# Kernel optimization log

Measured on AMD Instinct MI355X. Metric: run time of the kernel, lower is better.

Reference implementation:

```python
import jax, jax.numpy as jnp
import numpy as np

B, DIN, DOUT = 4096, 4096, 4096

def setup_inputs() -> dict:
    key = jax.random.key(0)
    k1, k2, k3 = jax.random.split(key, 3)
    x = jax.random.normal(k1, (B, DIN), dtype=jnp.float32)
    W = jax.random.normal(k2, (DOUT, DIN), dtype=jnp.float32) * 0.01
    alpha = jnp.ones((DOUT, DIN), dtype=jnp.float32) * 0.01
    eta = jnp.asarray(0.1, dtype=jnp.float32)
    bias = jnp.zeros((DOUT,), dtype=jnp.float32)
    return {"x": x, "W": W, "alpha": alpha, "eta": eta, "bias": bias}

def reference(x, W, alpha, eta, bias):
    # y_slow = x @ W.T + b                          (B, DOUT)
    y_slow = jnp.einsum('bi,oi->bo', x, W) + bias
    # x_norm = x / (||x|| + 1e-8)
    x_norm = x / (jnp.linalg.norm(x, axis=-1, keepdims=True) + 1e-8)
    y_pre = jnp.tanh(y_slow)
    # plastic_i = eta * y_pre_i * sum_j sigmoid(alpha)_ij * x_norm_j * x_j
    # (algebraic rewrite of bmm over per-sample outer-product trace; same math)
    s = jnp.einsum('bi,oi->bo', x_norm * x, jax.nn.sigmoid(alpha))  # (B, DOUT)
    plastic = eta * y_pre * s
    return y_slow + plastic
```

## Files before the change

### kernel.cpp

```cpp
#include <hip/hip_runtime.h>
#include <hip/hip_bf16.h>
#include <math.h>


typedef __attribute__((ext_vector_type(4))) float floatx4;
typedef __attribute__((ext_vector_type(8))) short shortx8;

#define MAT_N 4096
#define MAT_ELEMS ((size_t)MAT_N * MAT_N)

__device__ __forceinline__ unsigned short f2bf(float f) {
    unsigned int u = __float_as_uint(f);
    unsigned int r = (u + 0x7fffu + ((u >> 16) & 1u)) >> 16;
    return (unsigned short)r;
}

__device__ __forceinline__ void gload_lds16(const void* gptr, void* lptr) {
    __builtin_amdgcn_global_load_lds(
        (const __attribute__((address_space(1))) unsigned int*)gptr,
        (__attribute__((address_space(3))) unsigned int*)lptr,
        16, 0, 0);
}

__global__ __launch_bounds__(512) void convx_kernel(const float* __restrict__ x,
                                                    unsigned short* __restrict__ xb,
                                                    unsigned char* __restrict__ p8,
                                                    float* __restrict__ sumsq) {
    size_t base = ((size_t)blockIdx.x * 512 + threadIdx.x) * 8;
    const float4* xp = (const float4*)(x + base);
    float4 a = xp[0], b = xp[1];
    float v[8] = {a.x, a.y, a.z, a.w, b.x, b.y, b.z, b.w};
    shortx8 xo;
    float sq[8];
    float s = 0.f;
#pragma unroll
    for (int j = 0; j < 8; j++) {
        xo[j] = (short)f2bf(v[j]);
        sq[j] = v[j] * v[j];
        s += sq[j];
    }
    *(shortx8*)(xb + base) = xo;
    int p0 = __builtin_amdgcn_cvt_pk_fp8_f32(sq[0], sq[1], 0, false);
    p0 = __builtin_amdgcn_cvt_pk_fp8_f32(sq[2], sq[3], p0, true);
    int p1 = __builtin_amdgcn_cvt_pk_fp8_f32(sq[4], sq[5], 0, false);
    p1 = __builtin_amdgcn_cvt_pk_fp8_f32(sq[6], sq[7], p1, true);
    int2 pv = {p0, p1};
    *(int2*)(p8 + base) = pv;
    for (int off = 32; off > 0; off >>= 1) s += __shfl_down(s, off, 64);
    if ((threadIdx.x & 63) == 0) atomicAdd(&sumsq[base >> 12], s);
}

__global__ __launch_bounds__(512) void convwa_kernel(const float* __restrict__ W,
                                                     const float* __restrict__ alpha,
                                                     unsigned short* __restrict__ wb,
                                                     unsigned char* __restrict__ a8) {
    size_t base = ((size_t)blockIdx.x * 512 + threadIdx.x) * 8;
    const float4* wp = (const float4*)(W + base);
    const float4* ap = (const float4*)(alpha + base);
    float4 w0 = wp[0], w1 = wp[1], a0 = ap[0], a1 = ap[1];
    float wv[8] = {w0.x, w0.y, w0.z, w0.w, w1.x, w1.y, w1.z, w1.w};
    float av[8] = {a0.x, a0.y, a0.z, a0.w, a1.x, a1.y, a1.z, a1.w};
    shortx8 wo;
    float sg[8];
#pragma unroll
    for (int j = 0; j < 8; j++) {
        wo[j] = (short)f2bf(wv[j]);
        sg[j] = 1.0f / (1.0f + __expf(-av[j]));
    }
    *(shortx8*)(wb + base) = wo;
    int p0 = __builtin_amdgcn_cvt_pk_fp8_f32(sg[0], sg[1], 0, false);
    p0 = __builtin_amdgcn_cvt_pk_fp8_f32(sg[2], sg[3], p0, true);
    int p1 = __builtin_amdgcn_cvt_pk_fp8_f32(sg[4], sg[5], 0, false);
    p1 = __builtin_amdgcn_cvt_pk_fp8_f32(sg[6], sg[7], p1, true);
    int2 pv = {p0, p1};
    *(int2*)(a8 + base) = pv;
}

__global__ __launch_bounds__(512, 4) void fused_gemm_kernel(
    const unsigned short* __restrict__ X,
    const unsigned short* __restrict__ Wb,
    const unsigned char* __restrict__ P8,
    const unsigned char* __restrict__ A8,
    const float* __restrict__ bias,
    const float* __restrict__ eta_p,
    const float* __restrict__ sumsq,
    float* __restrict__ out) {
    constexpr int K = MAT_N;
    constexpr int N = MAT_N;
    __shared__ __align__(16) unsigned short sX[128 * 64];
    __shared__ __align__(16) unsigned short sW[128 * 64];
    __shared__ __align__(16) unsigned char  sP[128 * 64];
    __shared__ __align__(16) unsigned char  sA[128 * 64];

    const int tid = threadIdx.x;
    const int row0 = blockIdx.y * 128;
    const int col0 = blockIdx.x * 128;
    const int lane = tid & 63;
    const int wave = tid >> 6;
    const int wm = (wave >> 1) * 32;
    const int wn = (wave & 1) * 64;
    const int quad = lane >> 4;
    const int l16 = lane & 15;

    floatx4 accY[2][4], accS[2][4];
#pragma unroll
    for (int i = 0; i < 2; i++)
#pragma unroll
        for (int j = 0; j < 4; j++) {
            accY[i][j] = (floatx4){0.f, 0.f, 0.f, 0.f};
            accS[i][j] = (floatx4){0.f, 0.f, 0.f, 0.f};
        }

    const int row_s = tid >> 3;
    const int kc_g  = (tid & 7) ^ (row_s & 7);
    const size_t arow = (size_t)(row0 + row_s) * K + kc_g * 8;
    const size_t brow = (size_t)(col0 + row_s) * K + kc_g * 8;
    const int r8 = tid >> 2;
    const int slot8 = (2 * (tid & 3)) ^ (r8 & 6);
    const size_t prow = (size_t)(row0 + r8) * K + slot8 * 8;
    const size_t qrow = (size_t)(col0 + r8) * K + slot8 * 8;

    for (int k0 = 0; k0 < K; k0 += 64) {
#pragma unroll
        for (int i = 0; i < 2; i++) {
            const size_t go = (size_t)i * 64 * K + k0;
            const int lo = i * 4096 + tid * 8;
            gload_lds16(X + arow + go, sX + lo);
            gload_lds16(Wb + brow + go, sW + lo);
        }
        gload_lds16(P8 + prow + k0, sP + tid * 16);
        gload_lds16(A8 + qrow + k0, sA + tid * 16);
        __syncthreads();

#pragma unroll
        for (int s = 0; s < 2; s++) {
            const int kcp = ((s * 4 + quad) ^ (l16 & 7)) * 8;
            const int lsp = ((s * 4 + quad) ^ (l16 & 6)) * 8;
            {
                shortx8 af[2], bfr[4];
#pragma unroll
                for (int i = 0; i < 2; i++)
                    af[i] = *(const shortx8*)(sX + (wm + i * 16 + l16) * 64 + kcp);
#pragma unroll
                for (int j = 0; j < 4; j++)
                    bfr[j] = *(const shortx8*)(sW + (wn + j * 16 + l16) * 64 + kcp);
#pragma unroll
                for (int i = 0; i < 2; i++)
#pragma unroll
                    for (int j = 0; j < 4; j++)
                        accY[i][j] = __builtin_amdgcn_mfma_f32_16x16x32_bf16(af[i], bfr[j], accY[i][j], 0, 0, 0);
            }
            {
                long ap[2], bp[4];
#pragma unroll
                for (int i = 0; i < 2; i++)
                    ap[i] = *(const long*)(sP + (wm + i * 16 + l16) * 64 + lsp);
#pragma unroll
                for (int j = 0; j < 4; j++)
                    bp[j] = *(const long*)(sA + (wn + j * 16 + l16) * 64 + lsp);
#pragma unroll
                for (int i = 0; i < 2; i++)
#pragma unroll
                    for (int j = 0; j < 4; j++)
                        accS[i][j] = __builtin_amdgcn_mfma_f32_16x16x32_fp8_fp8(ap[i], bp[j], accS[i][j], 0, 0, 0);
            }
        }
        __syncthreads();
    }

    const float eta = *eta_p;
#pragma unroll
    for (int i = 0; i < 2; i++) {
#pragma unroll
        for (int r = 0; r < 4; r++) {
            const int grow = row0 + wm + i * 16 + quad * 4 + r;
            const float invn = 1.0f / (sqrtf(sumsq[grow]) + 1e-8f);
#pragma unroll
            for (int j = 0; j < 4; j++) {
                const int gcol = col0 + wn + j * 16 + l16;
                float y = accY[i][j][r] + bias[gcol];
                float s = accS[i][j][r] * invn;
                out[(size_t)grow * N + gcol] = y + eta * tanhf(y) * s;
            }
        }
    }
}

extern "C" void kernel_launch(void* const* d_in, const int* in_sizes, int n_in,
                              void* d_out, int out_size, void* d_ws, size_t ws_size,
                              hipStream_t stream) {
    const float* x     = (const float*)d_in[0];
    const float* W     = (const float*)d_in[1];
    const float* alpha = (const float*)d_in[2];
    const float* eta   = (const float*)d_in[3];
    const float* bias  = (const float*)d_in[4];
    float* out = (float*)d_out;

    char* ws = (char*)d_ws;
    float* sumsq = (float*)ws;
    unsigned short* xb = (unsigned short*)(ws + 16384);
    unsigned short* wb = xb + MAT_ELEMS;
    unsigned char*  p8 = (unsigned char*)(wb + MAT_ELEMS);
    unsigned char*  a8 = p8 + MAT_ELEMS;

    hipMemsetAsync(sumsq, 0, MAT_N * sizeof(float), stream);
    convx_kernel<<<MAT_ELEMS / (8 * 512), 512, 0, stream>>>(x, xb, p8, sumsq);
    convwa_kernel<<<MAT_ELEMS / (8 * 512), 512, 0, stream>>>(W, alpha, wb, a8);

    dim3 grid(MAT_N / 128, MAT_N / 128);
    fused_gemm_kernel<<<grid, 512, 0, stream>>>(xb, wb, p8, a8, bias, eta, sumsq, out);
}
```

Before: 466.3 us.

## Fold row norm into fp8 operand and permute fp8 layout for wide LDS reads

The x conversion kernel becomes one block per row. It computes the row norm itself and writes x^2/||x|| into the fp8 buffer, which removes the memset, the atomics and the per-row normalization in the GEMM epilogue. The fp8 operands are stored with a permuted 8-byte chunk order so each lane fetches both k-substeps in one 16-byte LDS read, replacing two 8-byte reads. Pre-scaling by the inverse norm before fp8 quantization changes rounding behaviour. The new packing drops the previous XOR swizzle, which may add LDS bank conflicts.

```diff
diff --git a/kernel.cpp b/kernel.cpp
--- a/kernel.cpp
+++ b/kernel.cpp
@@ -5,6 +5,7 @@
 
 typedef __attribute__((ext_vector_type(4))) float floatx4;
 typedef __attribute__((ext_vector_type(8))) short shortx8;
+typedef __attribute__((ext_vector_type(2))) long longx2;
 
 #define MAT_N 4096
 #define MAT_ELEMS ((size_t)MAT_N * MAT_N)
@@ -13,6 +14,11 @@
     unsigned int u = __float_as_uint(f);
     unsigned int r = (u + 0x7fffu + ((u >> 16) & 1u)) >> 16;
     return (unsigned short)r;
+}
+
+__device__ __forceinline__ int pack_fp8x4(float a, float b, float c, float d) {
+    int p = __builtin_amdgcn_cvt_pk_fp8_f32(a, b, 0, false);
+    return __builtin_amdgcn_cvt_pk_fp8_f32(c, d, p, true);
 }
 
 __device__ __forceinline__ void gload_lds16(const void* gptr, void* lptr) {
@@ -22,39 +28,55 @@
         16, 0, 0);
 }
 
-__global__ __launch_bounds__(512) void convx_kernel(const float* __restrict__ x,
+__device__ __forceinline__ int perm8(int c) { return ((c & 3) << 1) | (c >> 2); }
+
+__global__ __launch_bounds__(256) void convx_kernel(const float* __restrict__ x,
                                                     unsigned short* __restrict__ xb,
-                                                    unsigned char* __restrict__ p8,
-                                                    float* __restrict__ sumsq) {
-    size_t base = ((size_t)blockIdx.x * 512 + threadIdx.x) * 8;
-    const float4* xp = (const float4*)(x + base);
-    float4 a = xp[0], b = xp[1];
-    float v[8] = {a.x, a.y, a.z, a.w, b.x, b.y, b.z, b.w};
-    shortx8 xo;
-    float sq[8];
+                                                    unsigned char* __restrict__ p8) {
+    const int row = blockIdx.x;
+    const int t = threadIdx.x;
+    const float* xr = x + (size_t)row * MAT_N;
+    float v[2][8];
     float s = 0.f;
 #pragma unroll
-    for (int j = 0; j < 8; j++) {
-        xo[j] = (short)f2bf(v[j]);
-        sq[j] = v[j] * v[j];
-        s += sq[j];
-    }
-    *(shortx8*)(xb + base) = xo;
-    int p0 = __builtin_amdgcn_cvt_pk_fp8_f32(sq[0], sq[1], 0, false);
-    p0 = __builtin_amdgcn_cvt_pk_fp8_f32(sq[2], sq[3], p0, true);
-    int p1 = __builtin_amdgcn_cvt_pk_fp8_f32(sq[4], sq[5], 0, false);
-    p1 = __builtin_amdgcn_cvt_pk_fp8_f32(sq[6], sq[7], p1, true);
-    int2 pv = {p0, p1};
-    *(int2*)(p8 + base) = pv;
+    for (int h = 0; h < 2; h++) {
+        const float4* p = (const float4*)(xr + (t + h * 256) * 8);
+        float4 a = p[0], b = p[1];
+        v[h][0] = a.x; v[h][1] = a.y; v[h][2] = a.z; v[h][3] = a.w;
+        v[h][4] = b.x; v[h][5] = b.y; v[h][6] = b.z; v[h][7] = b.w;
+#pragma unroll
+        for (int j = 0; j < 8; j++) s += v[h][j] * v[h][j];
+    }
     for (int off = 32; off > 0; off >>= 1) s += __shfl_down(s, off, 64);
-    if ((threadIdx.x & 63) == 0) atomicAdd(&sumsq[base >> 12], s);
+    __shared__ float red[4];
+    if ((t & 63) == 0) red[t >> 6] = s;
+    __syncthreads();
+    const float inv = 1.0f / (sqrtf(red[0] + red[1] + red[2] + red[3]) + 1e-8f);
+    unsigned short* xrow = xb + (size_t)row * MAT_N;
+    unsigned char* prow = p8 + (size_t)row * MAT_N;
+#pragma unroll
+    for (int h = 0; h < 2; h++) {
+        const int c = t + h * 256;
+        shortx8 xo;
+        float q[8];
+#pragma unroll
+        for (int j = 0; j < 8; j++) {
+            xo[j] = (short)f2bf(v[h][j]);
+            q[j] = v[h][j] * v[h][j] * inv;
+        }
+        *(shortx8*)(xrow + c * 8) = xo;
+        int2 pv = {pack_fp8x4(q[0], q[1], q[2], q[3]),
+                   pack_fp8x4(q[4], q[5], q[6], q[7])};
+        *(int2*)(prow + (c & ~7) * 8 + perm8(c & 7) * 8) = pv;
+    }
 }
 
 __global__ __launch_bounds__(512) void convwa_kernel(const float* __restrict__ W,
                                                      const float* __restrict__ alpha,
                                                      unsigned short* __restrict__ wb,
                                                      unsigned char* __restrict__ a8) {
-    size_t base = ((size_t)blockIdx.x * 512 + threadIdx.x) * 8;
+    const size_t c = (size_t)blockIdx.x * 512 + threadIdx.x;
+    const size_t base = c * 8;
     const float4* wp = (const float4*)(W + base);
     const float4* ap = (const float4*)(alpha + base);
     float4 w0 = wp[0], w1 = wp[1], a0 = ap[0], a1 = ap[1];
@@ -68,12 +90,9 @@
         sg[j] = 1.0f / (1.0f + __expf(-av[j]));
     }
     *(shortx8*)(wb + base) = wo;
-    int p0 = __builtin_amdgcn_cvt_pk_fp8_f32(sg[0], sg[1], 0, false);
-    p0 = __builtin_amdgcn_cvt_pk_fp8_f32(sg[2], sg[3], p0, true);
-    int p1 = __builtin_amdgcn_cvt_pk_fp8_f32(sg[4], sg[5], 0, false);
-    p1 = __builtin_amdgcn_cvt_pk_fp8_f32(sg[6], sg[7], p1, true);
-    int2 pv = {p0, p1};
-    *(int2*)(a8 + base) = pv;
+    int2 pv = {pack_fp8x4(sg[0], sg[1], sg[2], sg[3]),
+               pack_fp8x4(sg[4], sg[5], sg[6], sg[7])};
+    *(int2*)(a8 + (base & ~(size_t)63) + perm8((int)(c & 7)) * 8) = pv;
 }
 
 __global__ __launch_bounds__(512, 4) void fused_gemm_kernel(
@@ -83,7 +102,6 @@
     const unsigned char* __restrict__ A8,
     const float* __restrict__ bias,
     const float* __restrict__ eta_p,
-    const float* __restrict__ sumsq,
     float* __restrict__ out) {
     constexpr int K = MAT_N;
     constexpr int N = MAT_N;
@@ -116,9 +134,8 @@
     const size_t arow = (size_t)(row0 + row_s) * K + kc_g * 8;
     const size_t brow = (size_t)(col0 + row_s) * K + kc_g * 8;
     const int r8 = tid >> 2;
-    const int slot8 = (2 * (tid & 3)) ^ (r8 & 6);
-    const size_t prow = (size_t)(row0 + r8) * K + slot8 * 8;
-    const size_t qrow = (size_t)(col0 + r8) * K + slot8 * 8;
+    const size_t prow = (size_t)(row0 + r8) * K + (tid & 3) * 16;
+    const size_t qrow = (size_t)(col0 + r8) * K + (tid & 3) * 16;
 
     for (int k0 = 0; k0 < K; k0 += 64) {
 #pragma unroll
@@ -132,38 +149,38 @@
         gload_lds16(A8 + qrow + k0, sA + tid * 16);
         __syncthreads();
 
+        {
+            longx2 apv[2], bpv[4];
+#pragma unroll
+            for (int i = 0; i < 2; i++)
+                apv[i] = *(const longx2*)(sP + (wm + i * 16 + l16) * 64 + quad * 16);
+#pragma unroll
+            for (int j = 0; j < 4; j++)
+                bpv[j] = *(const longx2*)(sA + (wn + j * 16 + l16) * 64 + quad * 16);
+#pragma unroll
+            for (int s = 0; s < 2; s++)
+#pragma unroll
+                for (int i = 0; i < 2; i++)
+#pragma unroll
+                    for (int j = 0; j < 4; j++)
+                        accS[i][j] = __builtin_amdgcn_mfma_f32_16x16x32_fp8_fp8(
+                            apv[i][s], bpv[j][s], accS[i][j], 0, 0, 0);
+        }
 #pragma unroll
         for (int s = 0; s < 2; s++) {
             const int kcp = ((s * 4 + quad) ^ (l16 & 7)) * 8;
-            const int lsp = ((s * 4 + quad) ^ (l16 & 6)) * 8;
-            {
-                shortx8 af[2], bfr[4];
-#pragma unroll
-                for (int i = 0; i < 2; i++)
-                    af[i] = *(const shortx8*)(sX + (wm + i * 16 + l16) * 64 + kcp);
+            shortx8 af[2], bfr[4];
+#pragma unroll
+            for (int i = 0; i < 2; i++)
+                af[i] = *(const shortx8*)(sX + (wm + i * 16 + l16) * 64 + kcp);
+#pragma unroll
+            for (int j = 0; j < 4; j++)
+                bfr[j] = *(const shortx8*)(sW + (wn + j * 16 + l16) * 64 + kcp);
+#pragma unroll
+            for (int i = 0; i < 2; i++)
 #pragma unroll
                 for (int j = 0; j < 4; j++)
-                    bfr[j] = *(const shortx8*)(sW + (wn + j * 16 + l16) * 64 + kcp);
-#pragma unroll
-                for (int i = 0; i < 2; i++)
-#pragma unroll
-                    for (int j = 0; j < 4; j++)
-                        accY[i][j] = __builtin_amdgcn_mfma_f32_16x16x32_bf16(af[i], bfr[j], accY[i][j], 0, 0, 0);
-            }
-            {
-                long ap[2], bp[4];
-#pragma unroll
-                for (int i = 0; i < 2; i++)
-                    ap[i] = *(const long*)(sP + (wm + i * 16 + l16) * 64 + lsp);
-#pragma unroll
-                for (int j = 0; j < 4; j++)
-                    bp[j] = *(const long*)(sA + (wn + j * 16 + l16) * 64 + lsp);
-#pragma unroll
-                for (int i = 0; i < 2; i++)
-#pragma unroll
-                    for (int j = 0; j < 4; j++)
-                        accS[i][j] = __builtin_amdgcn_mfma_f32_16x16x32_fp8_fp8(ap[i], bp[j], accS[i][j], 0, 0, 0);
-            }
+                    accY[i][j] = __builtin_amdgcn_mfma_f32_16x16x32_bf16(af[i], bfr[j], accY[i][j], 0, 0, 0);
         }
         __syncthreads();
     }
@@ -174,13 +191,11 @@
 #pragma unroll
         for (int r = 0; r < 4; r++) {
             const int grow = row0 + wm + i * 16 + quad * 4 + r;
-            const float invn = 1.0f / (sqrtf(sumsq[grow]) + 1e-8f);
 #pragma unroll
             for (int j = 0; j < 4; j++) {
                 const int gcol = col0 + wn + j * 16 + l16;
                 float y = accY[i][j][r] + bias[gcol];
-                float s = accS[i][j][r] * invn;
-                out[(size_t)grow * N + gcol] = y + eta * tanhf(y) * s;
+                out[(size_t)grow * N + gcol] = y + eta * tanhf(y) * accS[i][j][r];
             }
         }
     }
@@ -196,17 +211,14 @@
     const float* bias  = (const float*)d_in[4];
     float* out = (float*)d_out;
 
-    char* ws = (char*)d_ws;
-    float* sumsq = (float*)ws;
-    unsigned short* xb = (unsigned short*)(ws + 16384);
+    unsigned short* xb = (unsigned short*)d_ws;
     unsigned short* wb = xb + MAT_ELEMS;
     unsigned char*  p8 = (unsigned char*)(wb + MAT_ELEMS);
     unsigned char*  a8 = p8 + MAT_ELEMS;
 
-    hipMemsetAsync(sumsq, 0, MAT_N * sizeof(float), stream);
-    convx_kernel<<<MAT_ELEMS / (8 * 512), 512, 0, stream>>>(x, xb, p8, sumsq);
+    convx_kernel<<<MAT_N, 256, 0, stream>>>(x, xb, p8);
     convwa_kernel<<<MAT_ELEMS / (8 * 512), 512, 0, stream>>>(W, alpha, wb, a8);
 
     dim3 grid(MAT_N / 128, MAT_N / 128);
-    fused_gemm_kernel<<<grid, 512, 0, stream>>>(xb, wb, p8, a8, bias, eta, sumsq, out);
-}
+    fused_gemm_kernel<<<grid, 512, 0, stream>>>(xb, wb, p8, a8, bias, eta, out);
+}
```

New measurement: 491.2 us. +5.3%, slower.
